# Performance work log

Hardware: AMD Instinct MI355X
Metric: run time of the kernel (lower is better)

## Reference

```python
import jax, jax.numpy as jnp
import numpy as np

B, T, D, H, L, P = 256, 96, 64, 256, 5, 14
H2 = 2 * H   # decoder hidden
O = D        # output_size must equal input_size (decoder feeds its own output back)


def setup_inputs() -> dict:
    key = jax.random.key(0)
    ks = iter(jax.random.split(key, 32))
    s = 0.08  # weight scale to keep gates out of saturation
    rn = lambda shape, sc=s: jax.random.normal(next(ks), shape, jnp.float32) * sc
    return dict(
        x=rn((B, T, D), 1.0),
        # encoder: bidirectional, layer 0 input=D, layers 1..4 input=2H
        enc_Wih0=rn((2, 4 * H, D)), enc_Whh0=rn((2, 4 * H, H)),
        enc_bih0=rn((2, 4 * H)), enc_bhh0=rn((2, 4 * H)),
        enc_Wih=rn((L - 1, 2, 4 * H, 2 * H)), enc_Whh=rn((L - 1, 2, 4 * H, H)),
        enc_bih=rn((L - 1, 2, 4 * H)), enc_bhh=rn((L - 1, 2, 4 * H)),
        # decoder: unidirectional, hidden=2H, layer 0 input=D, layers 1..4 input=2H
        dec_Wih0=rn((4 * H2, D)), dec_Whh0=rn((4 * H2, H2)),
        dec_bih0=rn((4 * H2,)), dec_bhh0=rn((4 * H2,)),
        dec_Wih=rn((L - 1, 4 * H2, H2)), dec_Whh=rn((L - 1, 4 * H2, H2)),
        dec_bih=rn((L - 1, 4 * H2)), dec_bhh=rn((L - 1, 4 * H2)),
        fc_W=rn((O, H2)), fc_b=rn((O,)),
    )


def _lstm_cell(x, h, c, Wih, Whh, bih, bhh):
    # PyTorch gate order: i, f, g, o
    g = x @ Wih.T + h @ Whh.T + (bih + bhh)
    i, f, gg, o = jnp.split(g, 4, axis=-1)
    c = jax.nn.sigmoid(f) * c + jax.nn.sigmoid(i) * jnp.tanh(gg)
    h = jax.nn.sigmoid(o) * jnp.tanh(c)
    return h, c


def _scan_dir(xs, Wih, Whh, bih, bhh, reverse):
    # xs: (T, B, Din); returns per-step hidden (T,B,Hn) + final (h, c)
    Bn, Hn = xs.shape[1], Whh.shape[-1]
    z = jnp.zeros((Bn, Hn), xs.dtype)

    def step(carry, xt):
        h, c = carry
        h, c = _lstm_cell(xt, h, c, Wih, Whh, bih, bhh)
        return (h, c), h

    (hT, cT), hs = jax.lax.scan(step, (z, z), xs, reverse=reverse)
    return hs, hT, cT


def _forward(x, enc_Wih0, enc_Whh0, enc_bih0, enc_bhh0,
             enc_Wih, enc_Whh, enc_bih, enc_bhh,
             dec_Wih0, dec_Whh0, dec_bih0, dec_bhh0,
             dec_Wih, dec_Whh, dec_bih, dec_bhh, fc_W, fc_b):
    xs = jnp.swapaxes(x, 0, 1)  # (T, B, D)
    inp = xs
    h_fin, c_fin = [], []
    for l in range(L):
        if l == 0:
            Wih, Whh, bih, bhh = enc_Wih0, enc_Whh0, enc_bih0, enc_bhh0
        else:
            Wih, Whh, bih, bhh = enc_Wih[l - 1], enc_Whh[l - 1], enc_bih[l - 1], enc_bhh[l - 1]
        hs_f, hTf, cTf = _scan_dir(inp, Wih[0], Whh[0], bih[0], bhh[0], False)
        hs_b, hTb, cTb = _scan_dir(inp, Wih[1], Whh[1], bih[1], bhh[1], True)
        inp = jnp.concatenate([hs_f, hs_b], axis=-1)  # (T, B, 2H)
        # matches h_n.view(L,2,B,H).transpose(1,2).view(L,B,2H): per layer [fwd, bwd]
        h_fin.append(jnp.concatenate([hTf, hTb], axis=-1))
        c_fin.append(jnp.concatenate([cTf, cTb], axis=-1))
    h0 = jnp.stack(h_fin)  # (L, B, 2H)
    c0 = jnp.stack(c_fin)

    dec_params = [(dec_Wih0, dec_Whh0, dec_bih0, dec_bhh0)] + \
                 [(dec_Wih[l], dec_Whh[l], dec_bih[l], dec_bhh[l]) for l in range(L - 1)]

    def dec_step(carry, _):
        h, c, xt = carry
        z = xt
        nh, nc = [], []
        for l, (Wih, Whh, bih, bhh) in enumerate(dec_params):
            hl, cl = _lstm_cell(z, h[l], c[l], Wih, Whh, bih, bhh)
            z = hl
            nh.append(hl); nc.append(cl)
        out = z @ fc_W.T + fc_b  # (B, O); fed back as next decoder input
        return (jnp.stack(nh), jnp.stack(nc), out), out

    _, outs = jax.lax.scan(dec_step, (h0, c0, x[:, -1, :]), None, length=P)
    return jnp.swapaxes(outs, 0, 1)  # (B, P, O)


def reference(x, enc_Wih0, enc_Whh0, enc_bih0, enc_bhh0,
              enc_Wih, enc_Whh, enc_bih, enc_bhh,
              dec_Wih0, dec_Whh0, dec_bih0, dec_bhh0,
              dec_Wih, dec_Whh, dec_bih, dec_bhh, fc_W, fc_b):
    return _forward(x, enc_Wih0, enc_Whh0, enc_bih0, enc_bhh0,
                    enc_Wih, enc_Whh, enc_bih, enc_bhh,
                    dec_Wih0, dec_Whh0, dec_bih0, dec_bhh0,
                    dec_Wih, dec_Whh, dec_bih, dec_bhh, fc_W, fc_b)
```

## Files before the change

kernel.cpp:

```cpp
#include <hip/hip_runtime.h>

typedef _Float16 f16;
using half8 = __attribute__((ext_vector_type(8))) _Float16;
using half4 = __attribute__((ext_vector_type(4))) _Float16;
using f32x4 = __attribute__((ext_vector_type(4))) float;

#define DEV __device__ __forceinline__
#define LD8(p) (*(const half8*)(const void*)(p))

DEV f32x4 mfma16(half8 a, half8 b, f32x4 c) {
  return __builtin_amdgcn_mfma_f32_16x16x32_f16(a, b, c, 0, 0, 0);
}
DEV float sigf(float x) { return 1.f / (1.f + __expf(-x)); }
DEV float tanhf2(float x) { float e = __expf(2.f * x); return 1.f - 2.f / (e + 1.f); }

static const size_t OFF_WIH0   = 0;
static const size_t OFF_WIH14  = 262144;
static const size_t OFF_WHH    = 8650752;
static const size_t OFF_WDEC0  = 13893632;
static const size_t OFF_WDEC14 = 16252928;
static const size_t OFF_WFC    = 33030144;
static const size_t OFF_X16    = 33095680;
static const size_t OFF_SEQA   = 36241408;
static const size_t OFF_SEQB   = 61407232;
static const size_t OFF_XG     = 86573056;
static const size_t OFF_HBUF   = 187236352;
static const size_t OFF_FLAGS  = 187760640;
static const size_t OFF_DHDB   = 188284928;
static const size_t OFF_DCST   = 190906368;
static const size_t OFF_ZFC    = 193527808;

__global__ __launch_bounds__(256) void prep(
    const float* __restrict__ x,
    const float* __restrict__ eWih0, const float* __restrict__ eWhh0,
    const float* __restrict__ eWih,  const float* __restrict__ eWhh,
    const float* __restrict__ dWih0, const float* __restrict__ dWhh0,
    const float* __restrict__ dWih,  const float* __restrict__ dWhh,
    const float* __restrict__ fcW,   char* __restrict__ ws)
{
  f16* wih0   = (f16*)(ws + OFF_WIH0);
  f16* wih14  = (f16*)(ws + OFF_WIH14);
  f16* whhf   = (f16*)(ws + OFF_WHH);
  f16* wdec0  = (f16*)(ws + OFF_WDEC0);
  f16* wdec14 = (f16*)(ws + OFF_WDEC14);
  f16* wfc    = (f16*)(ws + OFF_WFC);
  f16* x16    = (f16*)(ws + OFF_X16);
  f16* zfc    = (f16*)(ws + OFF_ZFC);
  int* flags  = (int*)(ws + OFF_FLAGS);
  const size_t total = 18137152;
  for (size_t i = (size_t)blockIdx.x * blockDim.x + threadIdx.x; i < total;
       i += (size_t)gridDim.x * blockDim.x) {
    size_t j = i;
    if (j < 131072) { wih0[j] = (f16)eWih0[j]; continue; }
    j -= 131072;
    if (j < 4194304) { wih14[j] = (f16)eWih[j]; continue; }
    j -= 4194304;
    if (j < 2621440) {
      size_t l = j >> 19, i2 = j & 524287;
      int d   = (int)(i2 >> 18);
      int uh  = (int)((i2 >> 17) & 1);
      int w   = (int)((i2 >> 14) & 7);
      int g   = (int)((i2 >> 12) & 3);
      int kc  = (int)((i2 >> 9) & 7);
      int lnv = (int)((i2 >> 3) & 63);
      int e   = (int)(i2 & 7);
      int unit = uh * 128 + w * 16 + (lnv & 15);
      int k = kc * 32 + (lnv >> 4) * 8 + e;
      int row = g * 256 + unit;
      float v = (l == 0) ? eWhh0[((size_t)d * 1024 + row) * 256 + k]
                         : eWhh[((((l - 1) * 2 + (size_t)d) * 1024) + row) * 256 + k];
      whhf[j] = (f16)v;
      continue;
    }
    j -= 2621440;
    if (j < 1179648) {
      size_t r = j / 576, c = j % 576;
      wdec0[j] = (f16)((c < 64) ? dWih0[r * 64 + c] : dWhh0[r * 512 + (c - 64)]);
      continue;
    }
    j -= 1179648;
    if (j < 8388608) {
      size_t l = j >> 21, rem = j & 2097151;
      size_t r = rem >> 10, c = rem & 1023;
      wdec14[j] = (f16)((c < 512) ? dWih[(l * 2048 + r) * 512 + c]
                                  : dWhh[(l * 2048 + r) * 512 + (c - 512)]);
      continue;
    }
    j -= 8388608;
    if (j < 32768) { wfc[j] = (f16)fcW[j]; continue; }
    j -= 32768;
    if (j < 1572864) {
      size_t t = j >> 14, rem = j & 16383;
      size_t b = rem >> 6, d = rem & 63;
      x16[j] = (f16)x[(b * 96 + t) * 64 + d];
      continue;
    }
    j -= 1572864;
    if (j < 16384) {
      size_t b = j >> 6, d = j & 63;
      zfc[b * 512 + d] = (f16)x[(b * 96 + 95) * 64 + d];
      continue;
    }
    j -= 16384;
    flags[j] = 0;
  }
}

__global__ __launch_bounds__(256) void gemm_xg(
    const f16* __restrict__ A, int K, const f16* __restrict__ W,
    const float* __restrict__ bih, const float* __restrict__ bhh,
    f16* __restrict__ xg)
{
  __shared__ __align__(16) f16 As[128 * 32];
  __shared__ __align__(16) f16 Ws[128 * 32];
  const int dir = blockIdx.y >> 3;
  const int cb  = (blockIdx.y & 7) * 128;
  const int rb  = blockIdx.x * 128;
  const int tid = threadIdx.x;
  const int wv = tid >> 6, ln = tid & 63;
  const int wr = wv >> 1, wc = wv & 1;
  const f16* Wd = W + (size_t)dir * 1024 * K;

  f32x4 acc[4][4];
#pragma unroll
  for (int m = 0; m < 4; m++)
#pragma unroll
    for (int n = 0; n < 4; n++) acc[m][n] = (f32x4){0.f, 0.f, 0.f, 0.f};

  const int sr = tid >> 1;
  const int sk = (tid & 1) * 16;
  const int nk = K >> 5;
  for (int kt = 0; kt < nk; ++kt) {
    half8 va0 = LD8(&A[(size_t)(rb + sr) * K + kt * 32 + sk]);
    half8 va1 = LD8(&A[(size_t)(rb + sr) * K + kt * 32 + sk + 8]);
    half8 vw0 = LD8(&Wd[(size_t)(cb + sr) * K + kt * 32 + sk]);
    half8 vw1 = LD8(&Wd[(size_t)(cb + sr) * K + kt * 32 + sk + 8]);
    *(half8*)&As[sr * 32 + sk] = va0;
    *(half8*)&As[sr * 32 + sk + 8] = va1;
    *(half8*)&Ws[sr * 32 + sk] = vw0;
    *(half8*)&Ws[sr * 32 + sk + 8] = vw1;
    __syncthreads();
    half8 af[4], bf[4];
#pragma unroll
    for (int m = 0; m < 4; m++)
      af[m] = LD8(&As[(wr * 64 + m * 16 + (ln & 15)) * 32 + (ln >> 4) * 8]);
#pragma unroll
    for (int n = 0; n < 4; n++)
      bf[n] = LD8(&Ws[(wc * 64 + n * 16 + (ln & 15)) * 32 + (ln >> 4) * 8]);
#pragma unroll
    for (int m = 0; m < 4; m++)
#pragma unroll
      for (int n = 0; n < 4; n++) acc[m][n] = mfma16(af[m], bf[n], acc[m][n]);
    __syncthreads();
  }
#pragma unroll
  for (int n = 0; n < 4; n++) {
    const int col = cb + wc * 64 + n * 16 + (ln & 15);
    const float bsum = bih[dir * 1024 + col] + bhh[dir * 1024 + col];
    const int c16 = (cb + wc * 64 + n * 16) >> 4;
#pragma unroll
    for (int m = 0; m < 4; m++) {
      const int r16 = (rb + wr * 64 + m * 16) >> 4;
      half4 h;
#pragma unroll
      for (int r = 0; r < 4; r++) h[r] = (f16)(acc[m][n][r] + bsum);
      *(half4*)&xg[(((size_t)dir * 1536 + r16) * 64 + c16) * 256 + ln * 4] = h;
    }
  }
}

__global__ __launch_bounds__(512, 2) void enc_layer(
    const f16* __restrict__ xg, const f16* __restrict__ whhf,
    f16* __restrict__ hbuf, int* __restrict__ flags,
    f16* __restrict__ seqo, f16* __restrict__ hfin, float* __restrict__ cfin,
    int layer)
{
  const int bb = blockIdx.x;
  const int d = blockIdx.y >> 1, uh = blockIdx.y & 1;
  const int tid = threadIdx.x;
  const int wv = tid >> 6, ln = tid & 63;
  const int lc = ln & 15, lk = ln >> 4;

  __shared__ __align__(16) char hl[2][4096];

  half8 wfr[32];
  const f16* wbase = whhf + (((size_t)(d * 2 + uh) * 8 + wv) * 16384);
#pragma unroll
  for (int g = 0; g < 4; g++) {
#pragma unroll
    for (int jj = 0; jj < 4; jj++) {
      wfr[g * 8 + jj]     = LD8(&wbase[(size_t)(g * 8 + uh * 4 + jj) * 512 + ln * 8]);
      wfr[g * 8 + 4 + jj] = LD8(&wbase[(size_t)(g * 8 + (1 - uh) * 4 + jj) * 512 + ln * 8]);
    }
  }

  f16* hown = hbuf + ((size_t)((bb * 2 + d) * 2 + uh)) * 4096;
  const f16* hpart = hbuf + ((size_t)((bb * 2 + d) * 2 + (uh ^ 1))) * 4096;
  int* myflag = &flags[(bb * 2 + d) * 2 + uh];
  int* pflag  = &flags[(bb * 2 + d) * 2 + (uh ^ 1)];
  const int base = layer * 96;
  const int rowbase = bb * 16;
  const int unit_local = wv * 16 + lc;
  const int cu = uh * 128 + unit_local;

  f32x4 cst = (f32x4){0.f, 0.f, 0.f, 0.f};

#pragma unroll 2
  for (int t = 0; t < 96; ++t) {
    const int tt = d ? 95 - t : t;
    const int par = (t - 1) & 1, par2 = t & 1;
    f32x4 acc[4];
    const int r16 = tt * 16 + bb;
#pragma unroll
    for (int g = 0; g < 4; g++) {
      half4 v = *(const half4*)&xg[(((size_t)d * 1536 + r16) * 64 +
                                    (g * 16 + uh * 8 + wv)) * 256 + ln * 4];
      acc[g] = (f32x4){(float)v[0], (float)v[1], (float)v[2], (float)v[3]};
    }
    if (t > 0) {
      unsigned spin = 0;
      while (__hip_atomic_load(pflag, __ATOMIC_RELAXED,
                               __HIP_MEMORY_SCOPE_AGENT) < base + t) {
        if (++spin > 32768u) break;
      }
      asm volatile("" ::: "memory");
      unsigned long long q[4][2];
#pragma unroll
      for (int j = 0; j < 4; j++) {
        const f16* p = &hpart[par * 2048 + lc * 128 + j * 32 + lk * 8];
        q[j][0] = __hip_atomic_load((const unsigned long long*)p,
                                    __ATOMIC_RELAXED, __HIP_MEMORY_SCOPE_AGENT);
        q[j][1] = __hip_atomic_load((const unsigned long long*)(p + 4),
                                    __ATOMIC_RELAXED, __HIP_MEMORY_SCOPE_AGENT);
      }
      half8 ao[4];
#pragma unroll
      for (int j = 0; j < 4; j++) {
        int ba = (lc * 256 + j * 64 + lk * 16) ^ ((lc & 7) << 4);
        ao[j] = *(const half8*)&hl[par][ba];
      }
#pragma unroll
      for (int g = 0; g < 4; g++)
#pragma unroll
        for (int j = 0; j < 4; j++)
          acc[g] = mfma16(ao[j], wfr[g * 8 + j], acc[g]);
#pragma unroll
      for (int j = 0; j < 4; j++) {
        union { unsigned long long uq[2]; half8 h; } u;
        u.uq[0] = q[j][0]; u.uq[1] = q[j][1];
#pragma unroll
        for (int g = 0; g < 4; g++)
          acc[g] = mfma16(u.h, wfr[g * 8 + 4 + j], acc[g]);
      }
    }
    f16 hv[4];
#pragma unroll
    for (int r = 0; r < 4; r++) {
      float gi = sigf(acc[0][r]);
      float gf = sigf(acc[1][r]);
      float gg = tanhf2(acc[2][r]);
      float go = sigf(acc[3][r]);
      float cn = gf * cst[r] + gi * gg;
      cst[r] = cn;
      hv[r] = (f16)(go * tanhf2(cn));
    }
#pragma unroll
    for (int r = 0; r < 4; r++) {
      int row = lk * 4 + r;
      int ba = (row * 256 + unit_local * 2) ^ ((row & 7) << 4);
      *(f16*)&hl[par2][ba] = hv[r];
    }
    __syncthreads();
    {
      const int row = tid >> 5, c8 = tid & 31;
      int ba = (row * 256 + c8 * 8) ^ ((row & 7) << 4);
      unsigned long long v = *(const unsigned long long*)&hl[par2][ba];
      __hip_atomic_store((unsigned long long*)&hown[par2 * 2048 + row * 128 + c8 * 4],
                         v, __ATOMIC_RELAXED, __HIP_MEMORY_SCOPE_AGENT);
      *(unsigned long long*)&seqo[(size_t)tt * 131072 +
          (size_t)(rowbase + row) * 512 + d * 256 + uh * 128 + c8 * 4] = v;
      if (t == 95)
        *(unsigned long long*)&hfin[(size_t)(rowbase + row) * 512 +
                                    d * 256 + uh * 128 + c8 * 4] = v;
    }
    if (t == 95) {
#pragma unroll
      for (int r = 0; r < 4; r++)
        cfin[(size_t)(rowbase + lk * 4 + r) * 512 + d * 256 + cu] = cst[r];
    }
    asm volatile("s_waitcnt vmcnt(0)" ::: "memory");
    __syncthreads();
    if (tid == 0)
      __hip_atomic_store(myflag, base + t + 1, __ATOMIC_RELAXED,
                         __HIP_MEMORY_SCOPE_AGENT);
  }
}

__global__ __launch_bounds__(128) void dec_step(
    const f16* __restrict__ A0, int K0, const f16* __restrict__ A1,
    const f16* __restrict__ W, int Kt,
    const float* __restrict__ bih, const float* __restrict__ bhh,
    float* __restrict__ cst, f16* __restrict__ h1)
{
  const int u0 = blockIdx.y * 32;
  const int rb = blockIdx.x * 16;
  const int wv = threadIdx.x >> 6, ln = threadIdx.x & 63;
  const int cu = u0 + wv * 16 + (ln & 15);
  f32x4 acc[4];
#pragma unroll
  for (int g = 0; g < 4; g++) {
    float b = bih[g * 512 + cu] + bhh[g * 512 + cu];
    acc[g] = (f32x4){b, b, b, b};
  }
  const int K0c = K0 >> 5, Ktc = Kt >> 5;
  for (int kc = 0; kc < Ktc; kc++) {
    const f16* Ap; int ko;
    if (kc < K0c) { Ap = A0; ko = kc * 32; }
    else          { Ap = A1; ko = (kc - K0c) * 32; }
    half8 a = LD8(&Ap[(size_t)(rb + (ln & 15)) * 512 + ko + (ln >> 4) * 8]);
#pragma unroll
    for (int g = 0; g < 4; g++) {
      half8 b = LD8(&W[(size_t)(g * 512 + cu) * Kt + kc * 32 + (ln >> 4) * 8]);
      acc[g] = mfma16(a, b, acc[g]);
    }
  }
#pragma unroll
  for (int r = 0; r < 4; r++) {
    const int row = rb + (ln >> 4) * 4 + r;
    float gi = sigf(acc[0][r]);
    float gf = sigf(acc[1][r]);
    float gg = tanhf2(acc[2][r]);
    float go = sigf(acc[3][r]);
    float cp = cst[(size_t)row * 512 + cu];
    float cn = gf * cp + gi * gg;
    cst[(size_t)row * 512 + cu] = cn;
    h1[(size_t)row * 512 + cu] = (f16)(go * tanhf2(cn));
  }
}

__global__ __launch_bounds__(64) void fc_kernel(
    const f16* __restrict__ hin, const f16* __restrict__ Wf,
    const float* __restrict__ bf, float* __restrict__ out,
    f16* __restrict__ zfc, int s)
{
  const int rb = blockIdx.x * 16;
  const int ln = threadIdx.x;
  f32x4 acc[4];
#pragma unroll
  for (int n = 0; n < 4; n++) acc[n] = (f32x4){0.f, 0.f, 0.f, 0.f};
#pragma unroll
  for (int kc = 0; kc < 16; kc++) {
    half8 a = LD8(&hin[(size_t)(rb + (ln & 15)) * 512 + kc * 32 + (ln >> 4) * 8]);
#pragma unroll
    for (int n = 0; n < 4; n++) {
      half8 b = LD8(&Wf[(size_t)(n * 16 + (ln & 15)) * 512 + kc * 32 + (ln >> 4) * 8]);
      acc[n] = mfma16(a, b, acc[n]);
    }
  }
#pragma unroll
  for (int n = 0; n < 4; n++) {
    const int col = n * 16 + (ln & 15);
    const float bb = bf[col];
#pragma unroll
    for (int r = 0; r < 4; r++) {
      const int row = rb + (ln >> 4) * 4 + r;
      float v = acc[n][r] + bb;
      out[(size_t)row * 896 + s * 64 + col] = v;
      zfc[(size_t)row * 512 + col] = (f16)v;
    }
  }
}

extern "C" void kernel_launch(void* const* d_in, const int* in_sizes, int n_in,
                              void* d_out, int out_size, void* d_ws, size_t ws_size,
                              hipStream_t stream) {
  char* ws = (char*)d_ws;
  const float* x     = (const float*)d_in[0];
  const float* eWih0 = (const float*)d_in[1];
  const float* eWhh0 = (const float*)d_in[2];
  const float* ebih0 = (const float*)d_in[3];
  const float* ebhh0 = (const float*)d_in[4];
  const float* eWih  = (const float*)d_in[5];
  const float* eWhh  = (const float*)d_in[6];
  const float* ebih  = (const float*)d_in[7];
  const float* ebhh  = (const float*)d_in[8];
  const float* dWih0 = (const float*)d_in[9];
  const float* dWhh0 = (const float*)d_in[10];
  const float* dbih0 = (const float*)d_in[11];
  const float* dbhh0 = (const float*)d_in[12];
  const float* dWih  = (const float*)d_in[13];
  const float* dWhh  = (const float*)d_in[14];
  const float* dbih  = (const float*)d_in[15];
  const float* dbhh  = (const float*)d_in[16];
  const float* fcW   = (const float*)d_in[17];
  const float* fcb   = (const float*)d_in[18];

  f16* xg    = (f16*)(ws + OFF_XG);
  f16* hbuf  = (f16*)(ws + OFF_HBUF);
  int* flags = (int*)(ws + OFF_FLAGS);
  f16* dhdb  = (f16*)(ws + OFF_DHDB);
  float* dcst = (float*)(ws + OFF_DCST);
  f16* zfc   = (f16*)(ws + OFF_ZFC);
  f16* seqA  = (f16*)(ws + OFF_SEQA);
  f16* seqB  = (f16*)(ws + OFF_SEQB);

  prep<<<dim3(2048), dim3(256), 0, stream>>>(x, eWih0, eWhh0, eWih, eWhh,
                                             dWih0, dWhh0, dWih, dWhh, fcW, ws);

  for (int l = 0; l < 5; ++l) {
    const f16* Ain = (l == 0) ? (f16*)(ws + OFF_X16) : ((l & 1) ? seqA : seqB);
    const int K = (l == 0) ? 64 : 512;
    const f16* Wih = (l == 0) ? (f16*)(ws + OFF_WIH0)
                              : (f16*)(ws + OFF_WIH14) + (size_t)(l - 1) * 2 * 1024 * 512;
    const float* bi = (l == 0) ? ebih0 : ebih + (size_t)(l - 1) * 2048;
    const float* bh = (l == 0) ? ebhh0 : ebhh + (size_t)(l - 1) * 2048;
    gemm_xg<<<dim3(192, 16), dim3(256), 0, stream>>>(Ain, K, Wih, bi, bh, xg);

    const f16* whhf_l = (f16*)(ws + OFF_WHH) + (size_t)l * 524288;
    f16* so = (l & 1) ? seqB : seqA;
    enc_layer<<<dim3(16, 4), dim3(512), 0, stream>>>(
        xg, whhf_l, hbuf, flags, so,
        dhdb + (size_t)l * 131072, dcst + (size_t)l * 131072, l);
  }

  for (int s = 0; s < 14; ++s) {
    const int p = s & 1;
    for (int l = 0; l < 5; ++l) {
      dec_step<<<dim3(16, 16), dim3(128), 0, stream>>>(
          (l == 0) ? zfc : dhdb + (size_t)(p ^ 1) * 655360 + (size_t)(l - 1) * 131072,
          (l == 0) ? 64 : 512,
          dhdb + (size_t)p * 655360 + (size_t)l * 131072,
          (l == 0) ? (f16*)(ws + OFF_WDEC0)
                   : (f16*)(ws + OFF_WDEC14) + (size_t)(l - 1) * 2048 * 1024,
          (l == 0) ? 576 : 1024,
          (l == 0) ? dbih0 : dbih + (size_t)(l - 1) * 2048,
          (l == 0) ? dbhh0 : dbhh + (size_t)(l - 1) * 2048,
          dcst + (size_t)l * 131072,
          dhdb + (size_t)(p ^ 1) * 655360 + (size_t)l * 131072);
    }
    fc_kernel<<<dim3(16), dim3(64), 0, stream>>>(
        dhdb + (size_t)(p ^ 1) * 655360 + 4 * 131072, (f16*)(ws + OFF_WFC), fcb,
        (float*)d_out, zfc, s);
  }
}
```

Baseline: 4.407 ms.

## Precompute own-half recurrent MFMA after flag release and retile decoder step

In the encoder recurrence, the contribution of the block's own hidden-state half is now computed right after the step's flag is published, not after waiting on the partner. This moves that work off the critical cross-block dependency chain, and the seqo/hfin stores are likewise deferred past the flag store. The weight registers are pinned with an asm barrier, occupancy is hinted via waves_per_eu, and the spin limit is raised. The decoder step kernel now processes 64 rows per block and reuses each loaded weight fragment across four row tiles, cutting W reloads but launching fewer blocks (64 instead of 256).

```diff
diff --git a/kernel.cpp b/kernel.cpp
--- a/kernel.cpp
+++ b/kernel.cpp
@@ -169,7 +169,8 @@
   }
 }
 
-__global__ __launch_bounds__(512, 2) void enc_layer(
+__global__ __launch_bounds__(512) __attribute__((amdgpu_waves_per_eu(2, 2)))
+void enc_layer(
     const f16* __restrict__ xg, const f16* __restrict__ whhf,
     f16* __restrict__ hbuf, int* __restrict__ flags,
     f16* __restrict__ seqo, f16* __restrict__ hfin, float* __restrict__ cfin,
@@ -193,6 +194,8 @@
       wfr[g * 8 + 4 + jj] = LD8(&wbase[(size_t)(g * 8 + (1 - uh) * 4 + jj) * 512 + ln * 8]);
     }
   }
+#pragma unroll
+  for (int i = 0; i < 32; i++) asm volatile("" : "+v"(wfr[i]));
 
   f16* hown = hbuf + ((size_t)((bb * 2 + d) * 2 + uh)) * 4096;
   const f16* hpart = hbuf + ((size_t)((bb * 2 + d) * 2 + (uh ^ 1))) * 4096;
@@ -202,26 +205,34 @@
   const int rowbase = bb * 16;
   const int unit_local = wv * 16 + lc;
   const int cu = uh * 128 + unit_local;
+  const int erow = tid >> 5, ec8 = tid & 31;
+  const int eba = (erow * 256 + ec8 * 8) ^ ((erow & 7) << 4);
 
   f32x4 cst = (f32x4){0.f, 0.f, 0.f, 0.f};
-
-#pragma unroll 2
+  f32x4 ownp[4];
+#pragma unroll
+  for (int g = 0; g < 4; g++) ownp[g] = (f32x4){0.f, 0.f, 0.f, 0.f};
+
   for (int t = 0; t < 96; ++t) {
     const int tt = d ? 95 - t : t;
     const int par = (t - 1) & 1, par2 = t & 1;
+    const int r16 = tt * 16 + bb;
+    half4 xv[4];
+#pragma unroll
+    for (int g = 0; g < 4; g++)
+      xv[g] = *(const half4*)&xg[(((size_t)d * 1536 + r16) * 64 +
+                                  (g * 16 + uh * 8 + wv)) * 256 + ln * 4];
     f32x4 acc[4];
-    const int r16 = tt * 16 + bb;
 #pragma unroll
     for (int g = 0; g < 4; g++) {
-      half4 v = *(const half4*)&xg[(((size_t)d * 1536 + r16) * 64 +
-                                    (g * 16 + uh * 8 + wv)) * 256 + ln * 4];
-      acc[g] = (f32x4){(float)v[0], (float)v[1], (float)v[2], (float)v[3]};
+#pragma unroll
+      for (int r = 0; r < 4; r++) acc[g][r] = ownp[g][r] + (float)xv[g][r];
     }
     if (t > 0) {
       unsigned spin = 0;
       while (__hip_atomic_load(pflag, __ATOMIC_RELAXED,
                                __HIP_MEMORY_SCOPE_AGENT) < base + t) {
-        if (++spin > 32768u) break;
+        if (++spin > 65536u) break;
       }
       asm volatile("" ::: "memory");
       unsigned long long q[4][2];
@@ -233,17 +244,6 @@
         q[j][1] = __hip_atomic_load((const unsigned long long*)(p + 4),
                                     __ATOMIC_RELAXED, __HIP_MEMORY_SCOPE_AGENT);
       }
-      half8 ao[4];
-#pragma unroll
-      for (int j = 0; j < 4; j++) {
-        int ba = (lc * 256 + j * 64 + lk * 16) ^ ((lc & 7) << 4);
-        ao[j] = *(const half8*)&hl[par][ba];
-      }
-#pragma unroll
-      for (int g = 0; g < 4; g++)
-#pragma unroll
-        for (int j = 0; j < 4; j++)
-          acc[g] = mfma16(ao[j], wfr[g * 8 + j], acc[g]);
 #pragma unroll
       for (int j = 0; j < 4; j++) {
         union { unsigned long long uq[2]; half8 h; } u;
@@ -271,28 +271,37 @@
       *(f16*)&hl[par2][ba] = hv[r];
     }
     __syncthreads();
-    {
-      const int row = tid >> 5, c8 = tid & 31;
-      int ba = (row * 256 + c8 * 8) ^ ((row & 7) << 4);
-      unsigned long long v = *(const unsigned long long*)&hl[par2][ba];
-      __hip_atomic_store((unsigned long long*)&hown[par2 * 2048 + row * 128 + c8 * 4],
-                         v, __ATOMIC_RELAXED, __HIP_MEMORY_SCOPE_AGENT);
-      *(unsigned long long*)&seqo[(size_t)tt * 131072 +
-          (size_t)(rowbase + row) * 512 + d * 256 + uh * 128 + c8 * 4] = v;
-      if (t == 95)
-        *(unsigned long long*)&hfin[(size_t)(rowbase + row) * 512 +
-                                    d * 256 + uh * 128 + c8 * 4] = v;
-    }
-    if (t == 95) {
-#pragma unroll
-      for (int r = 0; r < 4; r++)
-        cfin[(size_t)(rowbase + lk * 4 + r) * 512 + d * 256 + cu] = cst[r];
-    }
+    unsigned long long v = *(const unsigned long long*)&hl[par2][eba];
+    __hip_atomic_store((unsigned long long*)&hown[par2 * 2048 + erow * 128 + ec8 * 4],
+                       v, __ATOMIC_RELAXED, __HIP_MEMORY_SCOPE_AGENT);
     asm volatile("s_waitcnt vmcnt(0)" ::: "memory");
     __syncthreads();
     if (tid == 0)
       __hip_atomic_store(myflag, base + t + 1, __ATOMIC_RELAXED,
                          __HIP_MEMORY_SCOPE_AGENT);
+    *(unsigned long long*)&seqo[(size_t)tt * 131072 +
+        (size_t)(rowbase + erow) * 512 + d * 256 + uh * 128 + ec8 * 4] = v;
+    if (t == 95) {
+      *(unsigned long long*)&hfin[(size_t)(rowbase + erow) * 512 +
+                                  d * 256 + uh * 128 + ec8 * 4] = v;
+#pragma unroll
+      for (int r = 0; r < 4; r++)
+        cfin[(size_t)(rowbase + lk * 4 + r) * 512 + d * 256 + cu] = cst[r];
+    } else {
+      half8 ao[4];
+#pragma unroll
+      for (int j = 0; j < 4; j++) {
+        int ba = (lc * 256 + j * 64 + lk * 16) ^ ((lc & 7) << 4);
+        ao[j] = *(const half8*)&hl[par2][ba];
+      }
+#pragma unroll
+      for (int g = 0; g < 4; g++) {
+        f32x4 s = (f32x4){0.f, 0.f, 0.f, 0.f};
+#pragma unroll
+        for (int j = 0; j < 4; j++) s = mfma16(ao[j], wfr[g * 8 + j], s);
+        ownp[g] = s;
+      }
+    }
   }
 }
 
@@ -303,38 +312,47 @@
     float* __restrict__ cst, f16* __restrict__ h1)
 {
   const int u0 = blockIdx.y * 32;
-  const int rb = blockIdx.x * 16;
+  const int rb = blockIdx.x * 64;
   const int wv = threadIdx.x >> 6, ln = threadIdx.x & 63;
-  const int cu = u0 + wv * 16 + (ln & 15);
-  f32x4 acc[4];
+  const int lc = ln & 15, lk = ln >> 4;
+  const int cu = u0 + wv * 16 + lc;
+  f32x4 acc[4][4];
 #pragma unroll
   for (int g = 0; g < 4; g++) {
     float b = bih[g * 512 + cu] + bhh[g * 512 + cu];
-    acc[g] = (f32x4){b, b, b, b};
+#pragma unroll
+    for (int rr = 0; rr < 4; rr++) acc[rr][g] = (f32x4){b, b, b, b};
   }
   const int K0c = K0 >> 5, Ktc = Kt >> 5;
   for (int kc = 0; kc < Ktc; kc++) {
     const f16* Ap; int ko;
     if (kc < K0c) { Ap = A0; ko = kc * 32; }
     else          { Ap = A1; ko = (kc - K0c) * 32; }
-    half8 a = LD8(&Ap[(size_t)(rb + (ln & 15)) * 512 + ko + (ln >> 4) * 8]);
-#pragma unroll
-    for (int g = 0; g < 4; g++) {
-      half8 b = LD8(&W[(size_t)(g * 512 + cu) * Kt + kc * 32 + (ln >> 4) * 8]);
-      acc[g] = mfma16(a, b, acc[g]);
-    }
-  }
-#pragma unroll
-  for (int r = 0; r < 4; r++) {
-    const int row = rb + (ln >> 4) * 4 + r;
-    float gi = sigf(acc[0][r]);
-    float gf = sigf(acc[1][r]);
-    float gg = tanhf2(acc[2][r]);
-    float go = sigf(acc[3][r]);
-    float cp = cst[(size_t)row * 512 + cu];
-    float cn = gf * cp + gi * gg;
-    cst[(size_t)row * 512 + cu] = cn;
-    h1[(size_t)row * 512 + cu] = (f16)(go * tanhf2(cn));
+    half8 b[4];
+#pragma unroll
+    for (int g = 0; g < 4; g++)
+      b[g] = LD8(&W[(size_t)(g * 512 + cu) * Kt + kc * 32 + lk * 8]);
+#pragma unroll
+    for (int rr = 0; rr < 4; rr++) {
+      half8 a = LD8(&Ap[(size_t)(rb + rr * 16 + lc) * 512 + ko + lk * 8]);
+#pragma unroll
+      for (int g = 0; g < 4; g++) acc[rr][g] = mfma16(a, b[g], acc[rr][g]);
+    }
+  }
+#pragma unroll
+  for (int rr = 0; rr < 4; rr++) {
+#pragma unroll
+    for (int r = 0; r < 4; r++) {
+      const int row = rb + rr * 16 + lk * 4 + r;
+      float gi = sigf(acc[rr][0][r]);
+      float gf = sigf(acc[rr][1][r]);
+      float gg = tanhf2(acc[rr][2][r]);
+      float go = sigf(acc[rr][3][r]);
+      float cp = cst[(size_t)row * 512 + cu];
+      float cn = gf * cp + gi * gg;
+      cst[(size_t)row * 512 + cu] = cn;
+      h1[(size_t)row * 512 + cu] = (f16)(go * tanhf2(cn));
+    }
   }
 }
 
@@ -426,7 +444,7 @@
   for (int s = 0; s < 14; ++s) {
     const int p = s & 1;
     for (int l = 0; l < 5; ++l) {
-      dec_step<<<dim3(16, 16), dim3(128), 0, stream>>>(
+      dec_step<<<dim3(4, 16), dim3(128), 0, stream>>>(
           (l == 0) ? zfc : dhdb + (size_t)(p ^ 1) * 655360 + (size_t)(l - 1) * 131072,
           (l == 0) ? 64 : 512,
           dhdb + (size_t)p * 655360 + (size_t)l * 131072,
```

After: 4.279 ms. 1.03x faster.
